# Performance work log

Measured on AMD Instinct MI355X. Metric: run time of the kernel, lower is better.

## Reference

```python
import jax, jax.numpy as jnp
import numpy as np

N_NODES = 50000
N_EDGES = 1600000
IN_CH = 128
OUT_CH = 16
K_HOPS = 2


def setup_inputs() -> dict:
    key = jax.random.key(0)
    k1, k2, k3, k4 = jax.random.split(key, 4)
    x = jax.random.normal(k1, (N_NODES, IN_CH), dtype=jnp.float32)
    W = jax.random.normal(k2, (OUT_CH, IN_CH), dtype=jnp.float32) * 0.05
    edge_weight = jax.random.uniform(k3, (N_EDGES,), dtype=jnp.float32)
    edge_index = jax.random.randint(k4, (2, N_EDGES), 0, N_NODES, dtype=jnp.int64)
    return {"x": x, "W": W, "edge_weight": edge_weight,
            "edge_index": edge_index, "K": K_HOPS}


def reference(x, W, edge_weight, edge_index, K):
    N = x.shape[0]
    # --- gcn_norm with add_self_loops=True (fill_value = 1.0) ---
    loops = jnp.arange(N, dtype=edge_index.dtype)
    row = jnp.concatenate([edge_index[0], loops])  # source nodes
    col = jnp.concatenate([edge_index[1], loops])  # target nodes
    w = jnp.concatenate([edge_weight, jnp.ones((N,), dtype=x.dtype)])
    deg = jax.ops.segment_sum(w, col, num_segments=N)  # degree at targets
    dinv = jnp.where(deg > 0, jax.lax.rsqrt(deg), 0.0)
    norm = dinv[row] * w * dinv[col]  # [E+N]

    # --- K-hop propagation: h <- A_hat @ h (gather-scale-scatter) ---
    def hop(h, _):
        msgs = norm[:, None] * h[row]               # [E+N, F] gather + scale
        h = jax.ops.segment_sum(msgs, col, num_segments=N)  # scatter-add
        return h, None

    h, _ = jax.lax.scan(hop, x, None, length=K)

    # --- linear projection (bias=False) then log_softmax over classes ---
    logits = h @ W.T  # [N, out_channels]
    return jax.nn.log_softmax(logits, axis=1)
```

## Files before the change

kernel.cpp:

```cpp
#include <hip/hip_runtime.h>
#include <hip/hip_fp16.h>
#include <math.h>

#define IN_CH 128
#define OUT_CH 16
#define B 256
#define CH_H 2048
#define CH_P 4096
#define LSH 6
#define LNODES 64
#define MAXNL 1024
#define MAXGH 2048

__device__ __forceinline__ unsigned short f2h(float f) {
    __half h = __float2half(f);
    unsigned short u;
    __builtin_memcpy(&u, &h, 2);
    return u;
}
__device__ __forceinline__ float h2f(unsigned short u) {
    __half h;
    __builtin_memcpy(&h, &u, 2);
    return __half2float(h);
}

__device__ __forceinline__ void scan_nl(const unsigned* __restrict__ vals, unsigned* dst,
                                        unsigned* sums, int NL) {
    int tid = threadIdx.x;
    int b0 = tid * 4;
    unsigned v[4]; unsigned loc = 0;
#pragma unroll
    for (int q = 0; q < 4; ++q) { int i = b0 + q; v[q] = (i < NL) ? vals[i] : 0u; loc += v[q]; }
    sums[tid] = loc;
    __syncthreads();
    for (int off = 1; off < B; off <<= 1) {
        unsigned a = (tid >= off) ? sums[tid - off] : 0u;
        __syncthreads();
        sums[tid] += a;
        __syncthreads();
    }
    unsigned run = sums[tid] - loc;
#pragma unroll
    for (int q = 0; q < 4; ++q) { int i = b0 + q; if (i < NL) dst[i] = run; run += v[q]; }
    __syncthreads();
}

__global__ void __launch_bounds__(B) k_hist(const int* __restrict__ col,
                                            unsigned* __restrict__ bh, int E, int NL) {
    __shared__ unsigned hc[MAXNL];
    int tid = threadIdx.x;
    for (int i = tid; i < NL; i += B) hc[i] = 0u;
    __syncthreads();
    int base = blockIdx.x * CH_H;
    int end = base + CH_H < E ? base + CH_H : E;
    for (int e = base + tid; e < end; e += B)
        atomicAdd(&hc[col[e] >> LSH], 1u);
    __syncthreads();
    unsigned* out = bh + (size_t)blockIdx.x * NL;
    for (int i = tid; i < NL; i += B) out[i] = hc[i];
}

__global__ void __launch_bounds__(B) k_colscan(unsigned* __restrict__ bh,
                                               unsigned* __restrict__ tot, int G, int NL) {
    int j = blockIdx.x;
    __shared__ unsigned s[B];
    int tid = threadIdx.x;
    unsigned carry = 0;
    for (int g0 = 0; g0 < G; g0 += B) {
        __syncthreads();
        int g = g0 + tid;
        unsigned v = (g < G) ? bh[(size_t)g * NL + j] : 0u;
        s[tid] = v;
        __syncthreads();
        for (int off = 1; off < B; off <<= 1) {
            unsigned add = (tid >= off) ? s[tid - off] : 0u;
            __syncthreads();
            s[tid] += add;
            __syncthreads();
        }
        if (g < G) bh[(size_t)g * NL + j] = carry + s[tid] - v;
        carry += s[B - 1];
    }
    if (tid == 0) tot[j] = carry;
}

__global__ void __launch_bounds__(B)
k_place(const int* __restrict__ row, const int* __restrict__ col, const float* __restrict__ ew,
        const unsigned* __restrict__ bh, const unsigned* __restrict__ tot,
        uint2* __restrict__ rec, int E, int NL, int F) {
    __shared__ uint2 srec[CH_P];
    __shared__ unsigned short slf[CH_P];
    __shared__ unsigned gbase[MAXNL];
    __shared__ unsigned lscan[MAXNL];
    __shared__ unsigned lctr[MAXNL];
    __shared__ unsigned sums[B];
    int tid = threadIdx.x;
    int c = blockIdx.x;
    int base = c * CH_P;
    int end = base + CH_P < E ? base + CH_P : E;
    int cnt = end - base;

    scan_nl(tot, gbase, sums, NL);
    for (int i = tid; i < NL; i += B) lctr[i] = 0u;
    __syncthreads();
    for (int j = tid; j < cnt; j += B)
        atomicAdd(&lctr[col[base + j] >> LSH], 1u);
    __syncthreads();
    scan_nl(lctr, lscan, sums, NL);
    for (int i = tid; i < NL; i += B) lctr[i] = lscan[i];
    __syncthreads();
    for (int j = tid; j < cnt; j += B) {
        int e = base + j;
        int cc = col[e];
        int lf = cc >> LSH;
        unsigned pos = atomicAdd(&lctr[lf], 1u);
        srec[pos] = make_uint2(((unsigned)row[e] << 6) | (unsigned)(cc & (LNODES - 1)),
                               __float_as_uint(ew[e]));
        slf[pos] = (unsigned short)lf;
    }
    __syncthreads();
    const unsigned* myb = bh + (size_t)(c * F) * NL;
    for (int j = tid; j < cnt; j += B) {
        int lf = slf[j];
        unsigned outp = gbase[lf] + myb[lf] + ((unsigned)j - lscan[lf]);
        rec[outp] = srec[j];
    }
}

__global__ void __launch_bounds__(B)
k_sort2proj(const uint2* __restrict__ rec, const unsigned* __restrict__ tot,
            const float* __restrict__ x, const float* __restrict__ W,
            unsigned* __restrict__ rec2, unsigned* __restrict__ nptr,
            float* __restrict__ dinv, float* __restrict__ g0, int N, int NL) {
    __shared__ unsigned sums[B];
    __shared__ unsigned gbase[MAXNL];
    __shared__ unsigned hist[LNODES];
    __shared__ unsigned start[LNODES];
    __shared__ float dacc[LNODES];
    __shared__ float dloc[LNODES];
    __shared__ float sW[OUT_CH * 132];
    int l = blockIdx.x, tid = threadIdx.x;

    for (int i = tid; i < OUT_CH * IN_CH; i += B) {
        int o = i >> 7, k = i & 127;
        sW[o * 132 + k] = W[i];
    }
    scan_nl(tot, gbase, sums, NL);
    int seg = (int)gbase[l];
    int end = seg + (int)tot[l];
    if (tid < LNODES) { hist[tid] = 0u; dacc[tid] = 0.f; }
    __syncthreads();
    for (int j = seg + tid; j < end; j += B) {
        uint2 u = rec[j];
        int cc = (int)(u.x & (LNODES - 1));
        atomicAdd(&hist[cc], 1u);
        atomicAdd(&dacc[cc], __uint_as_float(u.y));
    }
    __syncthreads();
    if (tid < LNODES) {
        unsigned v = hist[tid];
        unsigned sum = v;
        for (int off = 1; off < LNODES; off <<= 1) {
            unsigned o = __shfl_up(sum, off, 64);
            if (tid >= off) sum += o;
        }
        unsigned st = (unsigned)seg + sum - v;
        start[tid] = st;
        float dn = rsqrtf(1.0f + dacc[tid]);
        dloc[tid] = dn;
        int n = l * LNODES + tid;
        if (n < N) { nptr[n] = st; dinv[n] = dn; }
    }
    if (l == NL - 1 && tid == 0) nptr[N] = (unsigned)end;
    __syncthreads();
    for (int j = seg + tid; j < end; j += B) {
        uint2 u = rec[j];
        int cc = (int)(u.x & (LNODES - 1));
        unsigned pos = atomicAdd(&start[cc], 1u);
        rec2[pos] = ((u.x >> 6) << 16) | (unsigned)f2h(__uint_as_float(u.y));
    }
    int o = tid & 15;
    for (int nl = tid >> 4; nl < LNODES; nl += 16) {
        int n = l * LNODES + nl;
        if (n >= N) break;
        const float* xr = x + (size_t)n * IN_CH;
        const float* wr = sW + o * 132;
        float acc = 0.0f;
#pragma unroll
        for (int k = 0; k < IN_CH; k += 4) {
            float4 xv = *reinterpret_cast<const float4*>(xr + k);
            float4 wv = *reinterpret_cast<const float4*>(wr + k);
            acc += xv.x * wv.x + xv.y * wv.y + xv.z * wv.z + xv.w * wv.w;
        }
        g0[(size_t)n * OUT_CH + o] = dloc[nl] * acc;
    }
}

template <bool FINAL>
__global__ void __launch_bounds__(B)
k_hop(const unsigned* __restrict__ rec2, const unsigned* __restrict__ nptr,
      const float* __restrict__ dinv, const float* __restrict__ gin,
      float* __restrict__ out, int N) {
    int t = blockIdx.x * B + threadIdx.x;
    int n = t >> 4, ch = t & 15;
    if (n >= N) return;
    int j0 = (int)nptr[n], j1 = (int)nptr[n + 1];
    float acc = 0.f;
    int j = j0;
    for (; j + 3 < j1; j += 4) {
        unsigned u0 = rec2[j], u1 = rec2[j + 1], u2 = rec2[j + 2], u3 = rec2[j + 3];
        acc += h2f((unsigned short)u0) * gin[(size_t)(u0 >> 16) * OUT_CH + ch]
             + h2f((unsigned short)u1) * gin[(size_t)(u1 >> 16) * OUT_CH + ch]
             + h2f((unsigned short)u2) * gin[(size_t)(u2 >> 16) * OUT_CH + ch]
             + h2f((unsigned short)u3) * gin[(size_t)(u3 >> 16) * OUT_CH + ch];
    }
    for (; j < j1; ++j) {
        unsigned u = rec2[j];
        acc += h2f((unsigned short)u) * gin[(size_t)(u >> 16) * OUT_CH + ch];
    }
    float d = dinv[n];
    float s = gin[(size_t)n * OUT_CH + ch] + acc;
    if (!FINAL) {
        out[(size_t)n * OUT_CH + ch] = d * d * s;
    } else {
        float v = d * s;
        float m = v;
#pragma unroll
        for (int off = 1; off < 16; off <<= 1) m = fmaxf(m, __shfl_xor(m, off, 16));
        float se = expf(v - m);
#pragma unroll
        for (int off = 1; off < 16; off <<= 1) se += __shfl_xor(se, off, 16);
        out[(size_t)n * OUT_CH + ch] = v - m - logf(se);
    }
}


__global__ void fb_deginit(float* deg, int N) {
    int i = blockIdx.x * blockDim.x + threadIdx.x;
    if (i < N) deg[i] = 1.0f;
}
__global__ void fb_deg(const int* __restrict__ col, const float* __restrict__ ew,
                       float* deg, int E) {
    int e = blockIdx.x * blockDim.x + threadIdx.x;
    if (e < E) atomicAdd(&deg[col[e]], ew[e]);
}
__global__ void fb_dinv(const float* __restrict__ deg, float* dinv, int N) {
    int i = blockIdx.x * blockDim.x + threadIdx.x;
    if (i < N) dinv[i] = rsqrtf(deg[i]);
}
__global__ void fb_proj(const float* __restrict__ x, const float* __restrict__ W,
                        float* __restrict__ y, int N) {
    __shared__ float sW[OUT_CH * 132];
    for (int i = threadIdx.x; i < OUT_CH * IN_CH; i += blockDim.x) {
        int o = i >> 7, k = i & 127;
        sW[o * 132 + k] = W[i];
    }
    __syncthreads();
    int t = threadIdx.x;
    int n = blockIdx.x * 16 + (t >> 4);
    int o = t & 15;
    if (n >= N) return;
    const float* xr = x + (size_t)n * IN_CH;
    const float* wr = sW + o * 132;
    float acc = 0.0f;
#pragma unroll
    for (int k = 0; k < IN_CH; k += 4) {
        float4 xv = *reinterpret_cast<const float4*>(xr + k);
        float4 wv = *reinterpret_cast<const float4*>(wr + k);
        acc += xv.x * wv.x + xv.y * wv.y + xv.z * wv.z + xv.w * wv.w;
    }
    y[(size_t)n * OUT_CH + o] = acc;
}
__global__ void fb_selfinit(const float* __restrict__ hin, const float* __restrict__ dinv,
                            float* __restrict__ hout, int N) {
    int idx = blockIdx.x * blockDim.x + threadIdx.x;
    if (idx < N * OUT_CH) {
        float d = dinv[idx >> 4];
        hout[idx] = d * d * hin[idx];
    }
}
__global__ void fb_scat(const int* __restrict__ row, const int* __restrict__ col,
                        const float* __restrict__ ew, const float* __restrict__ dinv,
                        const float* __restrict__ hin, float* __restrict__ hout, int E) {
    long long idx = (long long)blockIdx.x * blockDim.x + threadIdx.x;
    int e = (int)(idx >> 4);
    int c = (int)(idx & 15);
    if (e >= E) return;
    int r = row[e], cl = col[e];
    float nv = dinv[r] * ew[e] * dinv[cl];
    atomicAdd(&hout[(size_t)cl * OUT_CH + c], nv * hin[(size_t)r * OUT_CH + c]);
}
__global__ void fb_lsm(const float* __restrict__ h, float* __restrict__ out, int N) {
    int n = blockIdx.x * blockDim.x + threadIdx.x;
    if (n >= N) return;
    const float* hr = h + (size_t)n * OUT_CH;
    float v[OUT_CH];
#pragma unroll
    for (int i = 0; i < OUT_CH; i++) v[i] = hr[i];
    float m = v[0];
#pragma unroll
    for (int i = 1; i < OUT_CH; i++) m = fmaxf(m, v[i]);
    float s = 0.0f;
#pragma unroll
    for (int i = 0; i < OUT_CH; i++) s += expf(v[i] - m);
    float lse = m + logf(s);
    float* orow = out + (size_t)n * OUT_CH;
#pragma unroll
    for (int i = 0; i < OUT_CH; i++) orow[i] = v[i] - lse;
}


extern "C" void kernel_launch(void* const* d_in, const int* in_sizes, int n_in,
                              void* d_out, int out_size, void* d_ws, size_t ws_size,
                              hipStream_t stream) {
    const float* x  = (const float*)d_in[0];
    const float* W  = (const float*)d_in[1];
    const float* ew = (const float*)d_in[2];
    const int*   ei = (const int*)d_in[3];

    int N = in_sizes[0] / IN_CH;
    int E = in_sizes[2];
    const int* row = ei;
    const int* col = ei + E;

    auto al = [](size_t v) { return (v + 255) & ~(size_t)255; };
    size_t N16 = (size_t)N * OUT_CH;

    int NL  = (N + LNODES - 1) >> LSH;
    int G_H = (E + CH_H - 1) / CH_H;
    int G_P = (E + CH_P - 1) / CH_P;
    int F   = CH_P / CH_H;
    int gH  = (int)((N16 + B - 1) / B);

    size_t o_rec  = 0;
    size_t o_rec2 = o_rec  + al((size_t)E * 8);
    size_t o_bh   = o_rec2 + al((size_t)E * 4);
    size_t o_tot  = o_bh   + al((size_t)G_H * NL * 4);
    size_t o_nptr = o_tot  + al((size_t)NL * 4);
    size_t o_dinv = o_nptr + al((size_t)(N + 1) * 4);
    size_t o_g0   = o_dinv + al((size_t)N * 4);
    size_t o_g1   = o_g0   + al(N16 * 4);
    size_t need   = o_g1   + al(N16 * 4);

    bool shape_ok = (NL <= MAXNL && G_H <= MAXGH && N <= 65536 &&
                     (G_P * F) <= G_H + F);

    char* ws = (char*)d_ws;

    if (shape_ok && need <= ws_size) {
        uint2*    rec  = (uint2*)(ws + o_rec);
        unsigned* rec2 = (unsigned*)(ws + o_rec2);
        unsigned* bh   = (unsigned*)(ws + o_bh);
        unsigned* tot  = (unsigned*)(ws + o_tot);
        unsigned* nptr = (unsigned*)(ws + o_nptr);
        float*    dinv = (float*)(ws + o_dinv);
        float*    g0   = (float*)(ws + o_g0);
        float*    g1   = (float*)(ws + o_g1);

        k_hist     <<<G_H, B, 0, stream>>>(col, bh, E, NL);
        k_colscan  <<<NL,  B, 0, stream>>>(bh, tot, G_H, NL);
        k_place    <<<G_P, B, 0, stream>>>(row, col, ew, bh, tot, rec, E, NL, F);
        k_sort2proj<<<NL,  B, 0, stream>>>(rec, tot, x, W, rec2, nptr, dinv, g0, N, NL);
        k_hop<false><<<gH, B, 0, stream>>>(rec2, nptr, dinv, g0, g1, N);
        k_hop<true ><<<gH, B, 0, stream>>>(rec2, nptr, dinv, g1, (float*)d_out, N);
    } else {
        size_t f_deg  = 0;
        size_t f_dinv = f_deg  + al((size_t)N * 4);
        size_t f_h0   = f_dinv + al((size_t)N * 4);
        size_t f_h1   = f_h0   + al(N16 * 4);
        float* deg  = (float*)(ws + f_deg);
        float* dinv = (float*)(ws + f_dinv);
        float* h0   = (float*)(ws + f_h0);
        float* h1   = (float*)(ws + f_h1);

        int gN   = (N + B - 1) / B;
        int gE   = (E + B - 1) / B;
        int gN16 = (N * OUT_CH + B - 1) / B;
        long long scat = (long long)E * OUT_CH;
        int gScat = (int)((scat + B - 1) / B);

        fb_deginit<<<gN, B, 0, stream>>>(deg, N);
        fb_deg<<<gE, B, 0, stream>>>(col, ew, deg, E);
        fb_dinv<<<gN, B, 0, stream>>>(deg, dinv, N);
        fb_proj<<<(N + 15) / 16, B, 0, stream>>>(x, W, h0, N);
        float* hin = h0; float* hout = h1;
        for (int k = 0; k < 2; k++) {
            fb_selfinit<<<gN16, B, 0, stream>>>(hin, dinv, hout, N);
            fb_scat<<<gScat, B, 0, stream>>>(row, col, ew, dinv, hin, hout, E);
            float* t = hin; hin = hout; hout = t;
        }
        fb_lsm<<<gN, B, 0, stream>>>(hin, (float*)d_out, N);
    }
}
```

Measured before the change: 124.4 us.

## Split per-bucket histogram into separate kernel with four sub-blocks per bucket

```diff
diff --git a/kernel.cpp b/kernel.cpp
--- a/kernel.cpp
+++ b/kernel.cpp
@@ -9,6 +9,7 @@
 #define CH_P 4096
 #define LSH 6
 #define LNODES 64
+#define S2 4
 #define MAXNL 1024
 #define MAXGH 2048
 
@@ -128,55 +129,84 @@
 }
 
 __global__ void __launch_bounds__(B)
+k_hist2(const uint2* __restrict__ rec, const unsigned* __restrict__ tot,
+        unsigned* __restrict__ h2, float* __restrict__ h2w, int NL) {
+    __shared__ unsigned sums[B];
+    __shared__ unsigned gbase[MAXNL];
+    __shared__ unsigned hist[LNODES];
+    __shared__ float wsum[LNODES];
+    int l = blockIdx.x >> 2, s = blockIdx.x & (S2 - 1);
+    int tid = threadIdx.x;
+    scan_nl(tot, gbase, sums, NL);
+    int seg = (int)gbase[l];
+    int cnt = (int)tot[l];
+    int q = (cnt + S2 - 1) / S2;
+    if (tid < LNODES) { hist[tid] = 0u; wsum[tid] = 0.f; }
+    __syncthreads();
+    int j0 = s * q;
+    int j1 = (s + 1) * q < cnt ? (s + 1) * q : cnt;
+    for (int j = j0 + tid; j < j1; j += B) {
+        uint2 u = rec[seg + j];
+        int cc = (int)(u.x & (LNODES - 1));
+        atomicAdd(&hist[cc], 1u);
+        atomicAdd(&wsum[cc], __uint_as_float(u.y));
+    }
+    __syncthreads();
+    if (tid < LNODES) {
+        size_t o = (size_t)(l * S2 + s) * LNODES + tid;
+        h2[o] = hist[tid];
+        h2w[o] = wsum[tid];
+    }
+}
+
+__global__ void __launch_bounds__(B)
 k_sort2proj(const uint2* __restrict__ rec, const unsigned* __restrict__ tot,
+            const unsigned* __restrict__ h2, const float* __restrict__ h2w,
             const float* __restrict__ x, const float* __restrict__ W,
             unsigned* __restrict__ rec2, unsigned* __restrict__ nptr,
             float* __restrict__ dinv, float* __restrict__ g0, int N, int NL) {
     __shared__ unsigned sums[B];
     __shared__ unsigned gbase[MAXNL];
-    __shared__ unsigned hist[LNODES];
-    __shared__ unsigned start[LNODES];
-    __shared__ float dacc[LNODES];
+    __shared__ unsigned start2[S2 * LNODES];
     __shared__ float dloc[LNODES];
     __shared__ float sW[OUT_CH * 132];
     int l = blockIdx.x, tid = threadIdx.x;
 
     for (int i = tid; i < OUT_CH * IN_CH; i += B) {
-        int o = i >> 7, k = i & 127;
-        sW[o * 132 + k] = W[i];
+        sW[(i >> 7) * 132 + (i & 127)] = W[i];
     }
     scan_nl(tot, gbase, sums, NL);
     int seg = (int)gbase[l];
-    int end = seg + (int)tot[l];
-    if (tid < LNODES) { hist[tid] = 0u; dacc[tid] = 0.f; }
-    __syncthreads();
-    for (int j = seg + tid; j < end; j += B) {
-        uint2 u = rec[j];
-        int cc = (int)(u.x & (LNODES - 1));
-        atomicAdd(&hist[cc], 1u);
-        atomicAdd(&dacc[cc], __uint_as_float(u.y));
-    }
-    __syncthreads();
+    int cnt = (int)tot[l];
     if (tid < LNODES) {
-        unsigned v = hist[tid];
-        unsigned sum = v;
+        size_t ho = (size_t)l * S2 * LNODES + tid;
+        unsigned c0 = h2[ho], c1 = h2[ho + LNODES], c2 = h2[ho + 2 * LNODES], c3 = h2[ho + 3 * LNODES];
+        float wv = h2w[ho] + h2w[ho + LNODES] + h2w[ho + 2 * LNODES] + h2w[ho + 3 * LNODES];
+        unsigned totn = c0 + c1 + c2 + c3;
+        unsigned sum = totn;
         for (int off = 1; off < LNODES; off <<= 1) {
             unsigned o = __shfl_up(sum, off, 64);
             if (tid >= off) sum += o;
         }
-        unsigned st = (unsigned)seg + sum - v;
-        start[tid] = st;
-        float dn = rsqrtf(1.0f + dacc[tid]);
+        unsigned st = (unsigned)seg + sum - totn;
+        int n = l * LNODES + tid;
+        if (n < N) nptr[n] = st;
+        float dn = rsqrtf(1.0f + wv);
         dloc[tid] = dn;
-        int n = l * LNODES + tid;
-        if (n < N) { nptr[n] = st; dinv[n] = dn; }
-    }
-    if (l == NL - 1 && tid == 0) nptr[N] = (unsigned)end;
-    __syncthreads();
-    for (int j = seg + tid; j < end; j += B) {
-        uint2 u = rec[j];
+        if (n < N) dinv[n] = dn;
+        start2[0 * LNODES + tid] = st;
+        start2[1 * LNODES + tid] = st + c0;
+        start2[2 * LNODES + tid] = st + c0 + c1;
+        start2[3 * LNODES + tid] = st + c0 + c1 + c2;
+    }
+    if (l == NL - 1 && tid == 0) nptr[N] = (unsigned)(seg + cnt);
+    __syncthreads();
+    int q = (cnt + S2 - 1) / S2;
+    for (int j = tid; j < cnt; j += B) {
+        int s = j / q;
+        uint2 u = rec[seg + j];
         int cc = (int)(u.x & (LNODES - 1));
-        unsigned pos = atomicAdd(&start[cc], 1u);
+        unsigned pos = atomicAdd(&start2[s * LNODES + cc], 1u);
         rec2[pos] = ((u.x >> 6) << 16) | (unsigned)f2h(__uint_as_float(u.y));
     }
     int o = tid & 15;
@@ -252,8 +282,7 @@
                         float* __restrict__ y, int N) {
     __shared__ float sW[OUT_CH * 132];
     for (int i = threadIdx.x; i < OUT_CH * IN_CH; i += blockDim.x) {
-        int o = i >> 7, k = i & 127;
-        sW[o * 132 + k] = W[i];
+        sW[(i >> 7) * 132 + (i & 127)] = W[i];
     }
     __syncthreads();
     int t = threadIdx.x;
@@ -336,7 +365,9 @@
     size_t o_rec2 = o_rec  + al((size_t)E * 8);
     size_t o_bh   = o_rec2 + al((size_t)E * 4);
     size_t o_tot  = o_bh   + al((size_t)G_H * NL * 4);
-    size_t o_nptr = o_tot  + al((size_t)NL * 4);
+    size_t o_h2   = o_tot  + al((size_t)NL * 4);
+    size_t o_h2w  = o_h2   + al((size_t)NL * S2 * LNODES * 4);
+    size_t o_nptr = o_h2w  + al((size_t)NL * S2 * LNODES * 4);
     size_t o_dinv = o_nptr + al((size_t)(N + 1) * 4);
     size_t o_g0   = o_dinv + al((size_t)N * 4);
     size_t o_g1   = o_g0   + al(N16 * 4);
@@ -352,17 +383,20 @@
         unsigned* rec2 = (unsigned*)(ws + o_rec2);
         unsigned* bh   = (unsigned*)(ws + o_bh);
         unsigned* tot  = (unsigned*)(ws + o_tot);
+        unsigned* h2   = (unsigned*)(ws + o_h2);
+        float*    h2w  = (float*)(ws + o_h2w);
         unsigned* nptr = (unsigned*)(ws + o_nptr);
         float*    dinv = (float*)(ws + o_dinv);
         float*    g0   = (float*)(ws + o_g0);
         float*    g1   = (float*)(ws + o_g1);
 
-        k_hist     <<<G_H, B, 0, stream>>>(col, bh, E, NL);
-        k_colscan  <<<NL,  B, 0, stream>>>(bh, tot, G_H, NL);
-        k_place    <<<G_P, B, 0, stream>>>(row, col, ew, bh, tot, rec, E, NL, F);
-        k_sort2proj<<<NL,  B, 0, stream>>>(rec, tot, x, W, rec2, nptr, dinv, g0, N, NL);
-        k_hop<false><<<gH, B, 0, stream>>>(rec2, nptr, dinv, g0, g1, N);
-        k_hop<true ><<<gH, B, 0, stream>>>(rec2, nptr, dinv, g1, (float*)d_out, N);
+        k_hist     <<<G_H,     B, 0, stream>>>(col, bh, E, NL);
+        k_colscan  <<<NL,      B, 0, stream>>>(bh, tot, G_H, NL);
+        k_place    <<<G_P,     B, 0, stream>>>(row, col, ew, bh, tot, rec, E, NL, F);
+        k_hist2    <<<NL * S2, B, 0, stream>>>(rec, tot, h2, h2w, NL);
+        k_sort2proj<<<NL,      B, 0, stream>>>(rec, tot, h2, h2w, x, W, rec2, nptr, dinv, g0, N, NL);
+        k_hop<false><<<gH,     B, 0, stream>>>(rec2, nptr, dinv, g0, g1, N);
+        k_hop<true ><<<gH,     B, 0, stream>>>(rec2, nptr, dinv, g1, (float*)d_out, N);
     } else {
         size_t f_deg  = 0;
         size_t f_dinv = f_deg  + al((size_t)N * 4);
```

Result: slower. 128.2 us (+3.1%).
